# Performance work log

Hardware: AMD Instinct MI355X
Metric: run time of the kernel (lower is better)

Reference implementation:

```python
import jax, jax.numpy as jnp
import numpy as np

B, EEG_D, FMRI_D, BD, H, NC = 131072, 128, 64, 128, 4, 2
HD = BD // H  # head dim = 32
EPS = 1e-5

def layernorm(x, g, b):
    m = jnp.mean(x, axis=-1, keepdims=True)
    v = jnp.var(x, axis=-1, keepdims=True)
    return (x - m) * jax.lax.rsqrt(v + EPS) * g + b

def setup_inputs() -> dict:
    key = jax.random.key(0)
    ks = jax.random.split(key, 24)
    r = lambda i, shape, s=0.05: jax.random.normal(ks[i], shape, dtype=jnp.float32) * s
    return {
        'eeg_feats': jax.random.normal(ks[0], (B, EEG_D), dtype=jnp.float32),
        'fmri_feats': jax.random.normal(ks[1], (B, FMRI_D), dtype=jnp.float32),
        # projections (weights stored [in, out])
        'We': r(2, (EEG_D, BD)), 'be': jnp.zeros((BD,)),
        'ge': jnp.ones((BD,)), 'bge': jnp.zeros((BD,)),
        'Wf': r(3, (FMRI_D, BD)), 'bf': jnp.zeros((BD,)),
        'gf': jnp.ones((BD,)), 'bgf': jnp.zeros((BD,)),
        # multihead attention
        'Wq': r(4, (BD, BD)), 'bq': jnp.zeros((BD,)),
        'Wk': r(5, (BD, BD)), 'bk': jnp.zeros((BD,)),
        'Wv': r(6, (BD, BD)), 'bv': jnp.zeros((BD,)),
        'Wo': r(7, (BD, BD)), 'bo': jnp.zeros((BD,)),
        # learned fusion
        'fusion_logits': jnp.zeros((2,)),
        'temperature': jnp.ones(()),
        # classifier
        'Wc1': r(8, (BD, BD // 2)), 'bc1': jnp.zeros((BD // 2,)),
        'gc': jnp.ones((BD // 2,)), 'bgc': jnp.zeros((BD // 2,)),
        'Wc2': r(9, (BD // 2, NC)), 'bc2': jnp.zeros((NC,)),
    }

def reference(eeg_feats, fmri_feats, We, be, ge, bge, Wf, bf, gf, bgf,
              Wq, bq, Wk, bk, Wv, bv, Wo, bo, fusion_logits, temperature,
              Wc1, bc1, gc, bgc, Wc2, bc2):
    # modality projections: Linear + LN + GELU (dropout off at eval)
    eeg_p = jax.nn.gelu(layernorm(eeg_feats @ We + be, ge, bge), approximate=False)
    fmri_p = jax.nn.gelu(layernorm(fmri_feats @ Wf + bf, gf, bgf), approximate=False)

    # cross-attention: query = eeg_p (1 token), kv = [eeg_p, fmri_p] (2 tokens)
    seq = jnp.stack([eeg_p, fmri_p], axis=1)                 # [B, 2, BD]
    q = (eeg_p @ Wq + bq).reshape(B, H, HD)                  # [B, H, HD]
    k = (seq @ Wk + bk).reshape(B, 2, H, HD)
    v = (seq @ Wv + bv).reshape(B, 2, H, HD)
    scores = jnp.einsum('bhd,bkhd->bhk', q, k) / jnp.sqrt(jnp.float32(HD))
    attn = jax.nn.softmax(scores, axis=-1)                   # [B, H, 2]
    ctx = jnp.einsum('bhk,bkhd->bhd', attn, v).reshape(B, BD)
    eeg_enh = ctx @ Wo + bo                                  # [B, BD]

    # learned temperature-scaled fusion over [eeg_enhanced, fmri_proj]
    w = jax.nn.softmax(fusion_logits / temperature, axis=0)
    fused = w[0] * eeg_enh + w[1] * fmri_p                   # [B, BD]

    # classifier: Linear + LN + ReLU + Linear
    h = jax.nn.relu(layernorm(fused @ Wc1 + bc1, gc, bgc))
    logits = h @ Wc2 + bc2                                   # [B, NC]
    return logits
```

## Files before the change

kernel.cpp:

```cpp
#include <hip/hip_runtime.h>
#include <math.h>

#define EPS 1e-5f
#define SCALE 0.17677669529663687f

#define OFF_We  0
#define OFF_Wf  16384
#define OFF_Wq  24576
#define OFF_Wk  40960
#define OFF_Wv  57344
#define OFF_Wo  73728
#define OFF_Wc1 90112
#define PACK_TOTAL 98304

#define CHUNK 4096
#define NCHUNK 24
#define WAVES 16

typedef __bf16 bf16x8 __attribute__((ext_vector_type(8)));
typedef float f32x4 __attribute__((ext_vector_type(4)));
typedef unsigned short ushort_t;
typedef unsigned short ushortx4 __attribute__((ext_vector_type(4)));

__device__ __forceinline__ ushort_t f2bf(float x) {
    return __builtin_bit_cast(ushort_t, (__bf16)x);
}
__device__ __forceinline__ float bf2f(ushort_t v) {
    unsigned u = ((unsigned)v) << 16;
    return __builtin_bit_cast(float, u);
}

__device__ __forceinline__ ushort_t f2bf_sw(float x) {
    unsigned u = __builtin_bit_cast(unsigned, x);
    u = (u + 0x7fffu + ((u >> 16) & 1u)) >> 16;
    return (ushort_t)u;
}

#define DPPADD(x, ctrl) \
    ((x) + __builtin_bit_cast(float, __builtin_amdgcn_update_dpp( \
        __builtin_bit_cast(int, (x)), __builtin_bit_cast(int, (x)), (ctrl), 0xF, 0xF, false)))

__device__ __forceinline__ float rowsum16(float x) {
    x = DPPADD(x, 0x121);
    x = DPPADD(x, 0x122);
    x = DPPADD(x, 0x124);
    x = DPPADD(x, 0x128);
    return x;
}

__device__ __forceinline__ float gelu_fast(float x) {
    float x2 = x * x;
    float u = x * fmaf(0.07135481283f, x2, 1.5957691216f);
    float e = __expf(-u);
    return x * __builtin_amdgcn_rcpf(1.0f + e);
}

__global__ __launch_bounds__(256) void pack_all(
    const float* __restrict__ We, const float* __restrict__ Wf,
    const float* __restrict__ Wq, const float* __restrict__ Wk,
    const float* __restrict__ Wv, const float* __restrict__ Wo,
    const float* __restrict__ Wc1, ushort_t* __restrict__ ws)
{
    int o = blockIdx.x * 256 + threadIdx.x;
    if (o >= PACK_TOTAL) return;
    const float* W; int K, N, base;
    if (o < OFF_Wf)        { W = We;  K = 128; N = 128; base = OFF_We; }
    else if (o < OFF_Wq)   { W = Wf;  K = 64;  N = 128; base = OFF_Wf; }
    else if (o < OFF_Wk)   { W = Wq;  K = 128; N = 128; base = OFF_Wq; }
    else if (o < OFF_Wv)   { W = Wk;  K = 128; N = 128; base = OFF_Wk; }
    else if (o < OFF_Wo)   { W = Wv;  K = 128; N = 128; base = OFF_Wv; }
    else if (o < OFF_Wc1)  { W = Wo;  K = 128; N = 128; base = OFF_Wo; }
    else                   { W = Wc1; K = 128; N = 64;  base = OFF_Wc1; }
    int e = o - base;
    int j = e & 7, l = (e >> 3) & 63, rest = e >> 9;
    int KS = K >> 5;
    int s = rest % KS, t = rest / KS;
    int k = s * 32 + ((l >> 4) << 3) + j;
    int n = (t << 4) + (l & 15);
    ws[o] = f2bf_sw(W[k * N + n]);
}

template<int KS>
__device__ __forceinline__ void load_af(bf16x8 af[KS], const ushort_t* A, int lane)
{
    const int quad = lane >> 4, l16 = lane & 15;
    #pragma unroll
    for (int ks = 0; ks < KS; ++ks)
        af[ks] = *(const bf16x8*)(A + l16 * 136 + ks * 32 + quad * 8);
}

template<int KS, int NT>
__device__ __forceinline__ void mma_chunk(const bf16x8 af[KS], const ushort_t* sWb,
                                          f32x4* acc, int lane)
{
    #pragma unroll
    for (int t = 0; t < NT; ++t)
        #pragma unroll
        for (int ks = 0; ks < KS; ++ks) {
            bf16x8 bb = *(const bf16x8*)(sWb + ((t * KS + ks) * 64 + lane) * 8);
            acc[t] = __builtin_amdgcn_mfma_f32_16x16x32_bf16(af[ks], bb, acc[t], 0, 0, 0);
        }
}

__global__ __launch_bounds__(1024, 1) void fusion_stage(
    const float* __restrict__ eeg, const float* __restrict__ fmri,
    const float* __restrict__ be, const float* __restrict__ ge, const float* __restrict__ bge,
    const float* __restrict__ bfb, const float* __restrict__ gf, const float* __restrict__ bgf,
    const float* __restrict__ bq, const float* __restrict__ bk, const float* __restrict__ bv,
    const float* __restrict__ bo,
    const float* __restrict__ fusion_logits, const float* __restrict__ temperature,
    const float* __restrict__ bc1, const float* __restrict__ gc, const float* __restrict__ bgc,
    const float* __restrict__ Wc2, const float* __restrict__ bc2,
    const ushort_t* __restrict__ ws, float* __restrict__ out)
{
    __shared__ __align__(16) ushort_t sW[2][CHUNK];
    __shared__ __align__(16) ushort_t B1[WAVES][16 * 136];
    __shared__ __align__(16) ushort_t B2[WAVES][16 * 136];

    const int tid = threadIdx.x;
    const int wave = tid >> 6, lane = tid & 63;
    const int quad = lane >> 4, l16 = lane & 15;
    const int rowbase = blockIdx.x * (WAVES * 16) + wave * 16;
    ushort_t* b1 = B1[wave];
    ushort_t* b2 = B2[wave];

    auto prefetch = [&](int c) {
        if (wave < 8) {
            const char* g = (const char*)(ws + c * CHUNK) + wave * 1024 + lane * 16;
            char* l = (char*)(sW[c & 1]) + wave * 1024;
            __builtin_amdgcn_global_load_lds(
                (const __attribute__((address_space(1))) void*)g,
                (__attribute__((address_space(3))) void*)l, 16, 0, 0);
        }
    };

    int ck = 0;
    auto step = [&]() -> const ushort_t* {
        __syncthreads();
        if (ck + 1 < NCHUNK) prefetch(ck + 1);
        const ushort_t* p = sW[ck & 1];
        ++ck;
        return p;
    };

    prefetch(0);

    {
        const float4* src = (const float4*)(eeg + (size_t)rowbase * 128);
        #pragma unroll
        for (int i = 0; i < 8; ++i) {
            int idx = i * 64 + lane;
            float4 v = src[idx];
            int r = idx >> 5, k4 = (idx & 31) * 4;
            *(ushortx4*)&b1[r * 136 + k4] =
                (ushortx4){f2bf(v.x), f2bf(v.y), f2bf(v.z), f2bf(v.w)};
        }
        const float4* srcf = (const float4*)(fmri + (size_t)rowbase * 64);
        #pragma unroll
        for (int i = 0; i < 4; ++i) {
            int idx = i * 64 + lane;
            float4 v = srcf[idx];
            int r = idx >> 4, k4 = (idx & 15) * 4;
            *(ushortx4*)&b2[r * 136 + k4] =
                (ushortx4){f2bf(v.x), f2bf(v.y), f2bf(v.z), f2bf(v.w)};
        }
    }

    float meanS[4], rstdS[4];

    {
        bf16x8 afR[4]; load_af<4>(afR, b1, lane);
        f32x4 acc[8];
        #pragma unroll
        for (int nt = 0; nt < 8; ++nt) {
            float b = be[nt * 16 + l16];
            acc[nt] = (f32x4){b, b, b, b};
        }
        mma_chunk<4, 2>(afR, step(), acc + 0, lane);
        mma_chunk<4, 2>(afR, step(), acc + 2, lane);
        mma_chunk<4, 2>(afR, step(), acc + 4, lane);
        mma_chunk<4, 2>(afR, step(), acc + 6, lane);
        #pragma unroll
        for (int r = 0; r < 4; ++r) {
            float s = 0.f, ss = 0.f;
            #pragma unroll
            for (int nt = 0; nt < 8; ++nt) { float x = acc[nt][r]; s += x; ss = fmaf(x, x, ss); }
            s = rowsum16(s); ss = rowsum16(ss);
            float m = s * (1.f / 128.f);
            meanS[r] = m;
            rstdS[r] = rsqrtf(ss * (1.f / 128.f) - m * m + EPS);
        }
        #pragma unroll
        for (int nt = 0; nt < 8; ++nt) {
            float g = ge[nt * 16 + l16], bb = bge[nt * 16 + l16];
            #pragma unroll
            for (int r = 0; r < 4; ++r) {
                float x = (acc[nt][r] - meanS[r]) * rstdS[r] * g + bb;
                b1[(quad * 4 + r) * 136 + nt * 16 + l16] = f2bf(gelu_fast(x));
            }
        }
    }

    {
        bf16x8 afR[2]; load_af<2>(afR, b2, lane);
        f32x4 acc[8];
        #pragma unroll
        for (int nt = 0; nt < 8; ++nt) {
            float b = bfb[nt * 16 + l16];
            acc[nt] = (f32x4){b, b, b, b};
        }
        mma_chunk<2, 4>(afR, step(), acc + 0, lane);
        mma_chunk<2, 4>(afR, step(), acc + 4, lane);
        #pragma unroll
        for (int r = 0; r < 4; ++r) {
            float s = 0.f, ss = 0.f;
            #pragma unroll
            for (int nt = 0; nt < 8; ++nt) { float x = acc[nt][r]; s += x; ss = fmaf(x, x, ss); }
            s = rowsum16(s); ss = rowsum16(ss);
            float m = s * (1.f / 128.f);
            meanS[r] = m;
            rstdS[r] = rsqrtf(ss * (1.f / 128.f) - m * m + EPS);
        }
        #pragma unroll
        for (int nt = 0; nt < 8; ++nt) {
            float g = gf[nt * 16 + l16], bb = bgf[nt * 16 + l16];
            #pragma unroll
            for (int r = 0; r < 4; ++r) {
                float x = (acc[nt][r] - meanS[r]) * rstdS[r] * g + bb;
                b2[(quad * 4 + r) * 136 + nt * 16 + l16] = f2bf(gelu_fast(x));
            }
        }
    }

    bf16x8 afE[4]; load_af<4>(afE, b1, lane);
    bf16x8 afF[4]; load_af<4>(afF, b2, lane);

    f32x4 q[8];
    {
        #pragma unroll
        for (int nt = 0; nt < 8; ++nt) {
            float b = bq[nt * 16 + l16];
            q[nt] = (f32x4){b, b, b, b};
        }
        mma_chunk<4, 2>(afE, step(), q + 0, lane);
        mma_chunk<4, 2>(afE, step(), q + 2, lane);
        mma_chunk<4, 2>(afE, step(), q + 4, lane);
        mma_chunk<4, 2>(afE, step(), q + 6, lane);
    }

    float a0v[4][4];
    {
        float pd[4][4];
        #pragma unroll
        for (int h = 0; h < 4; ++h)
            #pragma unroll
            for (int r = 0; r < 4; ++r) pd[h][r] = 0.f;
        #pragma unroll
        for (int c = 0; c < 4; ++c) {
            const ushort_t* p = step();
            #pragma unroll
            for (int tl = 0; tl < 2; ++tl) {
                int nt = c * 2 + tl;
                f32x4 e = {0.f, 0.f, 0.f, 0.f}, f = {0.f, 0.f, 0.f, 0.f};
                #pragma unroll
                for (int ks = 0; ks < 4; ++ks) {
                    bf16x8 bb = *(const bf16x8*)(p + ((tl * 4 + ks) * 64 + lane) * 8);
                    e = __builtin_amdgcn_mfma_f32_16x16x32_bf16(afE[ks], bb, e, 0, 0, 0);
                    f = __builtin_amdgcn_mfma_f32_16x16x32_bf16(afF[ks], bb, f, 0, 0, 0);
                }
                int h = nt >> 1;
                #pragma unroll
                for (int r = 0; r < 4; ++r)
                    pd[h][r] = fmaf(q[nt][r], e[r] - f[r], pd[h][r]);
            }
        }
        #pragma unroll
        for (int h = 0; h < 4; ++h)
            #pragma unroll
            for (int r = 0; r < 4; ++r) {
                float d = rowsum16(pd[h][r]) * SCALE;
                a0v[h][r] = __builtin_amdgcn_rcpf(1.0f + __expf(-d));
            }
    }

    #pragma unroll
    for (int c = 0; c < 4; ++c) {
        const ushort_t* p = step();
        #pragma unroll
        for (int tl = 0; tl < 2; ++tl) {
            int nt = c * 2 + tl;
            float b = bv[nt * 16 + l16];
            f32x4 e = {b, b, b, b}, f = {b, b, b, b};
            #pragma unroll
            for (int ks = 0; ks < 4; ++ks) {
                bf16x8 bb = *(const bf16x8*)(p + ((tl * 4 + ks) * 64 + lane) * 8);
                e = __builtin_amdgcn_mfma_f32_16x16x32_bf16(afE[ks], bb, e, 0, 0, 0);
                f = __builtin_amdgcn_mfma_f32_16x16x32_bf16(afF[ks], bb, f, 0, 0, 0);
            }
            int h = nt >> 1;
            #pragma unroll
            for (int r = 0; r < 4; ++r) {
                float a0 = a0v[h][r];
                float c0 = a0 * e[r] + (1.0f - a0) * f[r];
                b1[(quad * 4 + r) * 136 + nt * 16 + l16] = f2bf(c0);
            }
        }
    }

    {
        bf16x8 afC[4]; load_af<4>(afC, b1, lane);
        f32x4 acc[8];
        #pragma unroll
        for (int nt = 0; nt < 8; ++nt) {
            float b = bo[nt * 16 + l16];
            acc[nt] = (f32x4){b, b, b, b};
        }
        mma_chunk<4, 2>(afC, step(), acc + 0, lane);
        mma_chunk<4, 2>(afC, step(), acc + 2, lane);
        mma_chunk<4, 2>(afC, step(), acc + 4, lane);
        mma_chunk<4, 2>(afC, step(), acc + 6, lane);
        float t = temperature[0];
        float dl = (fusion_logits[0] - fusion_logits[1]) / t;
        float w0 = __builtin_amdgcn_rcpf(1.0f + __expf(-dl));
        float w1 = 1.0f - w0;
        #pragma unroll
        for (int nt = 0; nt < 8; ++nt)
            #pragma unroll
            for (int r = 0; r < 4; ++r) {
                int off = (quad * 4 + r) * 136 + nt * 16 + l16;
                float fp = bf2f(b2[off]);
                b1[off] = f2bf(w0 * acc[nt][r] + w1 * fp);
            }
    }

    {
        bf16x8 afU[4]; load_af<4>(afU, b1, lane);
        f32x4 accH[4];
        #pragma unroll
        for (int nt = 0; nt < 4; ++nt) {
            float b = bc1[nt * 16 + l16];
            accH[nt] = (f32x4){b, b, b, b};
        }
        mma_chunk<4, 2>(afU, step(), accH + 0, lane);
        mma_chunk<4, 2>(afU, step(), accH + 2, lane);
        #pragma unroll
        for (int r = 0; r < 4; ++r) {
            float s = 0.f, ss = 0.f;
            #pragma unroll
            for (int nt = 0; nt < 4; ++nt) { float x = accH[nt][r]; s += x; ss = fmaf(x, x, ss); }
            s = rowsum16(s); ss = rowsum16(ss);
            float m = s * (1.f / 64.f);
            meanS[r] = m;
            rstdS[r] = rsqrtf(ss * (1.f / 64.f) - m * m + EPS);
        }
        float hv[4][4];
        #pragma unroll
        for (int nt = 0; nt < 4; ++nt) {
            float g = gc[nt * 16 + l16], bb = bgc[nt * 16 + l16];
            #pragma unroll
            for (int r = 0; r < 4; ++r) {
                float x = (accH[nt][r] - meanS[r]) * rstdS[r] * g + bb;
                hv[nt][r] = fmaxf(x, 0.0f);
            }
        }
        float w2v[4][2];
        #pragma unroll
        for (int nt = 0; nt < 4; ++nt) {
            float2 w = *(const float2*)&Wc2[(nt * 16 + l16) * 2];
            w2v[nt][0] = w.x; w2v[nt][1] = w.y;
        }
        float o0c = bc2[0], o1c = bc2[1];
        #pragma unroll
        for (int r = 0; r < 4; ++r) {
            float p0 = 0.f, p1 = 0.f;
            #pragma unroll
            for (int nt = 0; nt < 4; ++nt) {
                p0 = fmaf(hv[nt][r], w2v[nt][0], p0);
                p1 = fmaf(hv[nt][r], w2v[nt][1], p1);
            }
            p0 = rowsum16(p0); p1 = rowsum16(p1);
            if (l16 == 0) {
                int row = rowbase + quad * 4 + r;
                float2 o; o.x = p0 + o0c; o.y = p1 + o1c;
                *(float2*)&out[row * 2] = o;
            }
        }
    }
}

extern "C" void kernel_launch(void* const* d_in, const int* in_sizes, int n_in,
                              void* d_out, int out_size, void* d_ws, size_t ws_size,
                              hipStream_t stream) {
    const float* eeg  = (const float*)d_in[0];
    const float* fmri = (const float*)d_in[1];
    const float* We   = (const float*)d_in[2];
    const float* be   = (const float*)d_in[3];
    const float* ge   = (const float*)d_in[4];
    const float* bge  = (const float*)d_in[5];
    const float* Wf   = (const float*)d_in[6];
    const float* bf   = (const float*)d_in[7];
    const float* gf   = (const float*)d_in[8];
    const float* bgf  = (const float*)d_in[9];
    const float* Wq   = (const float*)d_in[10];
    const float* bq   = (const float*)d_in[11];
    const float* Wk   = (const float*)d_in[12];
    const float* bk   = (const float*)d_in[13];
    const float* Wv   = (const float*)d_in[14];
    const float* bv   = (const float*)d_in[15];
    const float* Wo   = (const float*)d_in[16];
    const float* bo   = (const float*)d_in[17];
    const float* fl   = (const float*)d_in[18];
    const float* temp = (const float*)d_in[19];
    const float* Wc1  = (const float*)d_in[20];
    const float* bc1  = (const float*)d_in[21];
    const float* gc   = (const float*)d_in[22];
    const float* bgc  = (const float*)d_in[23];
    const float* Wc2  = (const float*)d_in[24];
    const float* bc2  = (const float*)d_in[25];
    float* out = (float*)d_out;
    ushort_t* ws = (ushort_t*)d_ws;

    hipLaunchKernelGGL(pack_all, dim3((PACK_TOTAL + 255) / 256), dim3(256), 0, stream,
                       We, Wf, Wq, Wk, Wv, Wo, Wc1, ws);

    int B = in_sizes[0] / 128;
    int grid = B / (WAVES * 16);
    hipLaunchKernelGGL(fusion_stage, dim3(grid), dim3(1024), 0, stream,
                       eeg, fmri, be, ge, bge, bf, gf, bgf,
                       bq, bk, bv, bo, fl, temp, bc1, gc, bgc, Wc2, bc2,
                       ws, out);
}
```

Measured before the change: 216.6 us.

## Process 32 rows per wave with 8 waves to reuse weight fragments

Each wave now handles two 16-row tiles, and every B fragment read from LDS feeds two MFMAs instead of one. The block shrinks to 8 waves (512 threads) with the same rows per block, and all 8 waves take part in the weight prefetch. This halves LDS weight reads per row and halves the barriers per row, but doubles accumulator and fragment registers per wave, which risks spills or lower occupancy.

```diff
diff --git a/kernel.cpp b/kernel.cpp
--- a/kernel.cpp
+++ b/kernel.cpp
@@ -15,7 +15,7 @@
 
 #define CHUNK 4096
 #define NCHUNK 24
-#define WAVES 16
+#define WAVES 8
 
 typedef __bf16 bf16x8 __attribute__((ext_vector_type(8)));
 typedef float f32x4 __attribute__((ext_vector_type(4)));
@@ -90,19 +90,20 @@
 }
 
 template<int KS, int NT>
-__device__ __forceinline__ void mma_chunk(const bf16x8 af[KS], const ushort_t* sWb,
-                                          f32x4* acc, int lane)
+__device__ __forceinline__ void mma2(const bf16x8 a0[KS], const bf16x8 a1[KS],
+                                     const ushort_t* sWb, f32x4* c0, f32x4* c1, int lane)
 {
     #pragma unroll
     for (int t = 0; t < NT; ++t)
         #pragma unroll
         for (int ks = 0; ks < KS; ++ks) {
             bf16x8 bb = *(const bf16x8*)(sWb + ((t * KS + ks) * 64 + lane) * 8);
-            acc[t] = __builtin_amdgcn_mfma_f32_16x16x32_bf16(af[ks], bb, acc[t], 0, 0, 0);
-        }
-}
-
-__global__ __launch_bounds__(1024, 1) void fusion_stage(
+            c0[t] = __builtin_amdgcn_mfma_f32_16x16x32_bf16(a0[ks], bb, c0[t], 0, 0, 0);
+            c1[t] = __builtin_amdgcn_mfma_f32_16x16x32_bf16(a1[ks], bb, c1[t], 0, 0, 0);
+        }
+}
+
+__global__ __launch_bounds__(512, 1) void fusion_stage(
     const float* __restrict__ eeg, const float* __restrict__ fmri,
     const float* __restrict__ be, const float* __restrict__ ge, const float* __restrict__ bge,
     const float* __restrict__ bfb, const float* __restrict__ gf, const float* __restrict__ bgf,
@@ -114,24 +115,22 @@
     const ushort_t* __restrict__ ws, float* __restrict__ out)
 {
     __shared__ __align__(16) ushort_t sW[2][CHUNK];
-    __shared__ __align__(16) ushort_t B1[WAVES][16 * 136];
-    __shared__ __align__(16) ushort_t B2[WAVES][16 * 136];
+    __shared__ __align__(16) ushort_t B1[WAVES][32 * 136];
+    __shared__ __align__(16) ushort_t B2[WAVES][32 * 136];
 
     const int tid = threadIdx.x;
     const int wave = tid >> 6, lane = tid & 63;
     const int quad = lane >> 4, l16 = lane & 15;
-    const int rowbase = blockIdx.x * (WAVES * 16) + wave * 16;
+    const int rowbase = blockIdx.x * (WAVES * 32) + wave * 32;
     ushort_t* b1 = B1[wave];
     ushort_t* b2 = B2[wave];
 
     auto prefetch = [&](int c) {
-        if (wave < 8) {
-            const char* g = (const char*)(ws + c * CHUNK) + wave * 1024 + lane * 16;
-            char* l = (char*)(sW[c & 1]) + wave * 1024;
-            __builtin_amdgcn_global_load_lds(
-                (const __attribute__((address_space(1))) void*)g,
-                (__attribute__((address_space(3))) void*)l, 16, 0, 0);
-        }
+        const char* g = (const char*)(ws + c * CHUNK) + wave * 1024 + lane * 16;
+        char* l = (char*)(sW[c & 1]) + wave * 1024;
+        __builtin_amdgcn_global_load_lds(
+            (const __attribute__((address_space(1))) void*)g,
+            (__attribute__((address_space(3))) void*)l, 16, 0, 0);
     };
 
     int ck = 0;
@@ -148,7 +147,7 @@
     {
         const float4* src = (const float4*)(eeg + (size_t)rowbase * 128);
         #pragma unroll
-        for (int i = 0; i < 8; ++i) {
+        for (int i = 0; i < 16; ++i) {
             int idx = i * 64 + lane;
             float4 v = src[idx];
             int r = idx >> 5, k4 = (idx & 31) * 4;
@@ -157,7 +156,7 @@
         }
         const float4* srcf = (const float4*)(fmri + (size_t)rowbase * 64);
         #pragma unroll
-        for (int i = 0; i < 4; ++i) {
+        for (int i = 0; i < 8; ++i) {
             int idx = i * 64 + lane;
             float4 v = srcf[idx];
             int r = idx >> 4, k4 = (idx & 15) * 4;
@@ -166,121 +165,146 @@
         }
     }
 
-    float meanS[4], rstdS[4];
-
-    {
-        bf16x8 afR[4]; load_af<4>(afR, b1, lane);
-        f32x4 acc[8];
+    {
+        bf16x8 af0[4], af1[4];
+        load_af<4>(af0, b1, lane);
+        load_af<4>(af1, b1 + 16 * 136, lane);
+        f32x4 acc[2][8];
         #pragma unroll
         for (int nt = 0; nt < 8; ++nt) {
             float b = be[nt * 16 + l16];
-            acc[nt] = (f32x4){b, b, b, b};
-        }
-        mma_chunk<4, 2>(afR, step(), acc + 0, lane);
-        mma_chunk<4, 2>(afR, step(), acc + 2, lane);
-        mma_chunk<4, 2>(afR, step(), acc + 4, lane);
-        mma_chunk<4, 2>(afR, step(), acc + 6, lane);
-        #pragma unroll
-        for (int r = 0; r < 4; ++r) {
-            float s = 0.f, ss = 0.f;
-            #pragma unroll
-            for (int nt = 0; nt < 8; ++nt) { float x = acc[nt][r]; s += x; ss = fmaf(x, x, ss); }
-            s = rowsum16(s); ss = rowsum16(ss);
-            float m = s * (1.f / 128.f);
-            meanS[r] = m;
-            rstdS[r] = rsqrtf(ss * (1.f / 128.f) - m * m + EPS);
-        }
-        #pragma unroll
-        for (int nt = 0; nt < 8; ++nt) {
-            float g = ge[nt * 16 + l16], bb = bge[nt * 16 + l16];
+            acc[0][nt] = (f32x4){b, b, b, b};
+            acc[1][nt] = (f32x4){b, b, b, b};
+        }
+        mma2<4, 2>(af0, af1, step(), acc[0] + 0, acc[1] + 0, lane);
+        mma2<4, 2>(af0, af1, step(), acc[0] + 2, acc[1] + 2, lane);
+        mma2<4, 2>(af0, af1, step(), acc[0] + 4, acc[1] + 4, lane);
+        mma2<4, 2>(af0, af1, step(), acc[0] + 6, acc[1] + 6, lane);
+        #pragma unroll
+        for (int g = 0; g < 2; ++g) {
+            float meanS[4], rstdS[4];
             #pragma unroll
             for (int r = 0; r < 4; ++r) {
-                float x = (acc[nt][r] - meanS[r]) * rstdS[r] * g + bb;
-                b1[(quad * 4 + r) * 136 + nt * 16 + l16] = f2bf(gelu_fast(x));
-            }
-        }
-    }
-
-    {
-        bf16x8 afR[2]; load_af<2>(afR, b2, lane);
-        f32x4 acc[8];
+                float s = 0.f, ss = 0.f;
+                #pragma unroll
+                for (int nt = 0; nt < 8; ++nt) { float x = acc[g][nt][r]; s += x; ss = fmaf(x, x, ss); }
+                s = rowsum16(s); ss = rowsum16(ss);
+                float m = s * (1.f / 128.f);
+                meanS[r] = m;
+                rstdS[r] = rsqrtf(ss * (1.f / 128.f) - m * m + EPS);
+            }
+            #pragma unroll
+            for (int nt = 0; nt < 8; ++nt) {
+                float gg = ge[nt * 16 + l16], bb = bge[nt * 16 + l16];
+                #pragma unroll
+                for (int r = 0; r < 4; ++r) {
+                    float x = (acc[g][nt][r] - meanS[r]) * rstdS[r] * gg + bb;
+                    b1[(g * 16 + quad * 4 + r) * 136 + nt * 16 + l16] = f2bf(gelu_fast(x));
+                }
+            }
+        }
+    }
+
+    {
+        bf16x8 af0[2], af1[2];
+        load_af<2>(af0, b2, lane);
+        load_af<2>(af1, b2 + 16 * 136, lane);
+        f32x4 acc[2][8];
         #pragma unroll
         for (int nt = 0; nt < 8; ++nt) {
             float b = bfb[nt * 16 + l16];
-            acc[nt] = (f32x4){b, b, b, b};
-        }
-        mma_chunk<2, 4>(afR, step(), acc + 0, lane);
-        mma_chunk<2, 4>(afR, step(), acc + 4, lane);
-        #pragma unroll
-        for (int r = 0; r < 4; ++r) {
-            float s = 0.f, ss = 0.f;
-            #pragma unroll
-            for (int nt = 0; nt < 8; ++nt) { float x = acc[nt][r]; s += x; ss = fmaf(x, x, ss); }
-            s = rowsum16(s); ss = rowsum16(ss);
-            float m = s * (1.f / 128.f);
-            meanS[r] = m;
-            rstdS[r] = rsqrtf(ss * (1.f / 128.f) - m * m + EPS);
-        }
-        #pragma unroll
-        for (int nt = 0; nt < 8; ++nt) {
-            float g = gf[nt * 16 + l16], bb = bgf[nt * 16 + l16];
+            acc[0][nt] = (f32x4){b, b, b, b};
+            acc[1][nt] = (f32x4){b, b, b, b};
+        }
+        mma2<2, 4>(af0, af1, step(), acc[0] + 0, acc[1] + 0, lane);
+        mma2<2, 4>(af0, af1, step(), acc[0] + 4, acc[1] + 4, lane);
+        #pragma unroll
+        for (int g = 0; g < 2; ++g) {
+            float meanS[4], rstdS[4];
             #pragma unroll
             for (int r = 0; r < 4; ++r) {
-                float x = (acc[nt][r] - meanS[r]) * rstdS[r] * g + bb;
-                b2[(quad * 4 + r) * 136 + nt * 16 + l16] = f2bf(gelu_fast(x));
-            }
-        }
-    }
-
-    bf16x8 afE[4]; load_af<4>(afE, b1, lane);
-    bf16x8 afF[4]; load_af<4>(afF, b2, lane);
-
-    f32x4 q[8];
+                float s = 0.f, ss = 0.f;
+                #pragma unroll
+                for (int nt = 0; nt < 8; ++nt) { float x = acc[g][nt][r]; s += x; ss = fmaf(x, x, ss); }
+                s = rowsum16(s); ss = rowsum16(ss);
+                float m = s * (1.f / 128.f);
+                meanS[r] = m;
+                rstdS[r] = rsqrtf(ss * (1.f / 128.f) - m * m + EPS);
+            }
+            #pragma unroll
+            for (int nt = 0; nt < 8; ++nt) {
+                float gg = gf[nt * 16 + l16], bb = bgf[nt * 16 + l16];
+                #pragma unroll
+                for (int r = 0; r < 4; ++r) {
+                    float x = (acc[g][nt][r] - meanS[r]) * rstdS[r] * gg + bb;
+                    b2[(g * 16 + quad * 4 + r) * 136 + nt * 16 + l16] = f2bf(gelu_fast(x));
+                }
+            }
+        }
+    }
+
+    bf16x8 afE[2][4], afF[2][4];
+    load_af<4>(afE[0], b1, lane);
+    load_af<4>(afE[1], b1 + 16 * 136, lane);
+    load_af<4>(afF[0], b2, lane);
+    load_af<4>(afF[1], b2 + 16 * 136, lane);
+
+    f32x4 q[2][8];
     {
         #pragma unroll
         for (int nt = 0; nt < 8; ++nt) {
             float b = bq[nt * 16 + l16];
-            q[nt] = (f32x4){b, b, b, b};
-        }
-        mma_chunk<4, 2>(afE, step(), q + 0, lane);
-        mma_chunk<4, 2>(afE, step(), q + 2, lane);
-        mma_chunk<4, 2>(afE, step(), q + 4, lane);
-        mma_chunk<4, 2>(afE, step(), q + 6, lane);
-    }
-
-    float a0v[4][4];
-    {
-        float pd[4][4];
-        #pragma unroll
-        for (int h = 0; h < 4; ++h)
-            #pragma unroll
-            for (int r = 0; r < 4; ++r) pd[h][r] = 0.f;
+            q[0][nt] = (f32x4){b, b, b, b};
+            q[1][nt] = (f32x4){b, b, b, b};
+        }
+        mma2<4, 2>(afE[0], afE[1], step(), q[0] + 0, q[1] + 0, lane);
+        mma2<4, 2>(afE[0], afE[1], step(), q[0] + 2, q[1] + 2, lane);
+        mma2<4, 2>(afE[0], afE[1], step(), q[0] + 4, q[1] + 4, lane);
+        mma2<4, 2>(afE[0], afE[1], step(), q[0] + 6, q[1] + 6, lane);
+    }
+
+    float a0v[2][4][4];
+    {
+        float pd[2][4][4];
+        #pragma unroll
+        for (int g = 0; g < 2; ++g)
+            #pragma unroll
+            for (int h = 0; h < 4; ++h)
+                #pragma unroll
+                for (int r = 0; r < 4; ++r) pd[g][h][r] = 0.f;
         #pragma unroll
         for (int c = 0; c < 4; ++c) {
             const ushort_t* p = step();
             #pragma unroll
             for (int tl = 0; tl < 2; ++tl) {
                 int nt = c * 2 + tl;
-                f32x4 e = {0.f, 0.f, 0.f, 0.f}, f = {0.f, 0.f, 0.f, 0.f};
+                f32x4 e0 = {0.f, 0.f, 0.f, 0.f}, f0 = {0.f, 0.f, 0.f, 0.f};
+                f32x4 e1 = {0.f, 0.f, 0.f, 0.f}, f1 = {0.f, 0.f, 0.f, 0.f};
                 #pragma unroll
                 for (int ks = 0; ks < 4; ++ks) {
                     bf16x8 bb = *(const bf16x8*)(p + ((tl * 4 + ks) * 64 + lane) * 8);
-                    e = __builtin_amdgcn_mfma_f32_16x16x32_bf16(afE[ks], bb, e, 0, 0, 0);
-                    f = __builtin_amdgcn_mfma_f32_16x16x32_bf16(afF[ks], bb, f, 0, 0, 0);
+                    e0 = __builtin_amdgcn_mfma_f32_16x16x32_bf16(afE[0][ks], bb, e0, 0, 0, 0);
+                    f0 = __builtin_amdgcn_mfma_f32_16x16x32_bf16(afF[0][ks], bb, f0, 0, 0, 0);
+                    e1 = __builtin_amdgcn_mfma_f32_16x16x32_bf16(afE[1][ks], bb, e1, 0, 0, 0);
+                    f1 = __builtin_amdgcn_mfma_f32_16x16x32_bf16(afF[1][ks], bb, f1, 0, 0, 0);
                 }
                 int h = nt >> 1;
                 #pragma unroll
-                for (int r = 0; r < 4; ++r)
-                    pd[h][r] = fmaf(q[nt][r], e[r] - f[r], pd[h][r]);
-            }
-        }
-        #pragma unroll
-        for (int h = 0; h < 4; ++h)
-            #pragma unroll
-            for (int r = 0; r < 4; ++r) {
-                float d = rowsum16(pd[h][r]) * SCALE;
-                a0v[h][r] = __builtin_amdgcn_rcpf(1.0f + __expf(-d));
-            }
+                for (int r = 0; r < 4; ++r) {
+                    pd[0][h][r] = fmaf(q[0][nt][r], e0[r] - f0[r], pd[0][h][r]);
+                    pd[1][h][r] = fmaf(q[1][nt][r], e1[r] - f1[r], pd[1][h][r]);
+                }
+            }
+        }
+        #pragma unroll
+        for (int g = 0; g < 2; ++g)
+            #pragma unroll
+            for (int h = 0; h < 4; ++h)
+                #pragma unroll
+                for (int r = 0; r < 4; ++r) {
+                    float d = rowsum16(pd[g][h][r]) * SCALE;
+                    a0v[g][h][r] = __builtin_amdgcn_rcpf(1.0f + __expf(-d));
+                }
     }
 
     #pragma unroll
@@ -290,79 +314,73 @@
         for (int tl = 0; tl < 2; ++tl) {
             int nt = c * 2 + tl;
             float b = bv[nt * 16 + l16];
-            f32x4 e = {b, b, b, b}, f = {b, b, b, b};
+            f32x4 e0 = {b, b, b, b}, f0 = {b, b, b, b};
+            f32x4 e1 = {b, b, b, b}, f1 = {b, b, b, b};
             #pragma unroll
             for (int ks = 0; ks < 4; ++ks) {
                 bf16x8 bb = *(const bf16x8*)(p + ((tl * 4 + ks) * 64 + lane) * 8);
-                e = __builtin_amdgcn_mfma_f32_16x16x32_bf16(afE[ks], bb, e, 0, 0, 0);
-                f = __builtin_amdgcn_mfma_f32_16x16x32_bf16(afF[ks], bb, f, 0, 0, 0);
+                e0 = __builtin_amdgcn_mfma_f32_16x16x32_bf16(afE[0][ks], bb, e0, 0, 0, 0);
+                f0 = __builtin_amdgcn_mfma_f32_16x16x32_bf16(afF[0][ks], bb, f0, 0, 0, 0);
+                e1 = __builtin_amdgcn_mfma_f32_16x16x32_bf16(afE[1][ks], bb, e1, 0, 0, 0);
+                f1 = __builtin_amdgcn_mfma_f32_16x16x32_bf16(afF[1][ks], bb, f1, 0, 0, 0);
             }
             int h = nt >> 1;
             #pragma unroll
             for (int r = 0; r < 4; ++r) {
-                float a0 = a0v[h][r];
-                float c0 = a0 * e[r] + (1.0f - a0) * f[r];
+                float a00 = a0v[0][h][r];
+                float a01 = a0v[1][h][r];
+                float c0 = a00 * e0[r] + (1.0f - a00) * f0[r];
+                float c1 = a01 * e1[r] + (1.0f - a01) * f1[r];
                 b1[(quad * 4 + r) * 136 + nt * 16 + l16] = f2bf(c0);
-            }
-        }
-    }
-
-    {
-        bf16x8 afC[4]; load_af<4>(afC, b1, lane);
-        f32x4 acc[8];
+                b1[(16 + quad * 4 + r) * 136 + nt * 16 + l16] = f2bf(c1);
+            }
+        }
+    }
+
+    {
+        bf16x8 afC0[4], afC1[4];
+        load_af<4>(afC0, b1, lane);
+        load_af<4>(afC1, b1 + 16 * 136, lane);
+        f32x4 acc[2][8];
         #pragma unroll
         for (int nt = 0; nt < 8; ++nt) {
             float b = bo[nt * 16 + l16];
-            acc[nt] = (f32x4){b, b, b, b};
-        }
-        mma_chunk<4, 2>(afC, step(), acc + 0, lane);
-        mma_chunk<4, 2>(afC, step(), acc + 2, lane);
-        mma_chunk<4, 2>(afC, step(), acc + 4, lane);
-        mma_chunk<4, 2>(afC, step(), acc + 6, lane);
+            acc[0][nt] = (f32x4){b, b, b, b};
+            acc[1][nt] = (f32x4){b, b, b, b};
+        }
+        mma2<4, 2>(afC0, afC1, step(), acc[0] + 0, acc[1] + 0, lane);
+        mma2<4, 2>(afC0, afC1, step(), acc[0] + 2, acc[1] + 2, lane);
+        mma2<4, 2>(afC0, afC1, step(), acc[0] + 4, acc[1] + 4, lane);
+        mma2<4, 2>(afC0, afC1, step(), acc[0] + 6, acc[1] + 6, lane);
         float t = temperature[0];
         float dl = (fusion_logits[0] - fusion_logits[1]) / t;
         float w0 = __builtin_amdgcn_rcpf(1.0f + __expf(-dl));
         float w1 = 1.0f - w0;
         #pragma unroll
-        for (int nt = 0; nt < 8; ++nt)
-            #pragma unroll
-            for (int r = 0; r < 4; ++r) {
-                int off = (quad * 4 + r) * 136 + nt * 16 + l16;
-                float fp = bf2f(b2[off]);
-                b1[off] = f2bf(w0 * acc[nt][r] + w1 * fp);
-            }
-    }
-
-    {
-        bf16x8 afU[4]; load_af<4>(afU, b1, lane);
-        f32x4 accH[4];
+        for (int g = 0; g < 2; ++g)
+            #pragma unroll
+            for (int nt = 0; nt < 8; ++nt)
+                #pragma unroll
+                for (int r = 0; r < 4; ++r) {
+                    int off = (g * 16 + quad * 4 + r) * 136 + nt * 16 + l16;
+                    float fp = bf2f(b2[off]);
+                    b1[off] = f2bf(w0 * acc[g][nt][r] + w1 * fp);
+                }
+    }
+
+    {
+        bf16x8 afU0[4], afU1[4];
+        load_af<4>(afU0, b1, lane);
+        load_af<4>(afU1, b1 + 16 * 136, lane);
+        f32x4 accH[2][4];
         #pragma unroll
         for (int nt = 0; nt < 4; ++nt) {
             float b = bc1[nt * 16 + l16];
-            accH[nt] = (f32x4){b, b, b, b};
-        }
-        mma_chunk<4, 2>(afU, step(), accH + 0, lane);
-        mma_chunk<4, 2>(afU, step(), accH + 2, lane);
-        #pragma unroll
-        for (int r = 0; r < 4; ++r) {
-            float s = 0.f, ss = 0.f;
-            #pragma unroll
-            for (int nt = 0; nt < 4; ++nt) { float x = accH[nt][r]; s += x; ss = fmaf(x, x, ss); }
-            s = rowsum16(s); ss = rowsum16(ss);
-            float m = s * (1.f / 64.f);
-            meanS[r] = m;
-            rstdS[r] = rsqrtf(ss * (1.f / 64.f) - m * m + EPS);
-        }
-        float hv[4][4];
-        #pragma unroll
-        for (int nt = 0; nt < 4; ++nt) {
-            float g = gc[nt * 16 + l16], bb = bgc[nt * 16 + l16];
-            #pragma unroll
-            for (int r = 0; r < 4; ++r) {
-                float x = (accH[nt][r] - meanS[r]) * rstdS[r] * g + bb;
-                hv[nt][r] = fmaxf(x, 0.0f);
-            }
-        }
+            accH[0][nt] = (f32x4){b, b, b, b};
+            accH[1][nt] = (f32x4){b, b, b, b};
+        }
+        mma2<4, 2>(afU0, afU1, step(), accH[0] + 0, accH[1] + 0, lane);
+        mma2<4, 2>(afU0, afU1, step(), accH[0] + 2, accH[1] + 2, lane);
         float w2v[4][2];
         #pragma unroll
         for (int nt = 0; nt < 4; ++nt) {
@@ -371,18 +389,42 @@
         }
         float o0c = bc2[0], o1c = bc2[1];
         #pragma unroll
-        for (int r = 0; r < 4; ++r) {
-            float p0 = 0.f, p1 = 0.f;
+        for (int g = 0; g < 2; ++g) {
+            float meanS[4], rstdS[4];
+            #pragma unroll
+            for (int r = 0; r < 4; ++r) {
+                float s = 0.f, ss = 0.f;
+                #pragma unroll
+                for (int nt = 0; nt < 4; ++nt) { float x = accH[g][nt][r]; s += x; ss = fmaf(x, x, ss); }
+                s = rowsum16(s); ss = rowsum16(ss);
+                float m = s * (1.f / 64.f);
+                meanS[r] = m;
+                rstdS[r] = rsqrtf(ss * (1.f / 64.f) - m * m + EPS);
+            }
+            float hv[4][4];
             #pragma unroll
             for (int nt = 0; nt < 4; ++nt) {
-                p0 = fmaf(hv[nt][r], w2v[nt][0], p0);
-                p1 = fmaf(hv[nt][r], w2v[nt][1], p1);
-            }
-            p0 = rowsum16(p0); p1 = rowsum16(p1);
-            if (l16 == 0) {
-                int row = rowbase + quad * 4 + r;
-                float2 o; o.x = p0 + o0c; o.y = p1 + o1c;
-                *(float2*)&out[row * 2] = o;
+                float gg = gc[nt * 16 + l16], bb = bgc[nt * 16 + l16];
+                #pragma unroll
+                for (int r = 0; r < 4; ++r) {
+                    float x = (accH[g][nt][r] - meanS[r]) * rstdS[r] * gg + bb;
+                    hv[nt][r] = fmaxf(x, 0.0f);
+                }
+            }
+            #pragma unroll
+            for (int r = 0; r < 4; ++r) {
+                float p0 = 0.f, p1 = 0.f;
+                #pragma unroll
+                for (int nt = 0; nt < 4; ++nt) {
+                    p0 = fmaf(hv[nt][r], w2v[nt][0], p0);
+                    p1 = fmaf(hv[nt][r], w2v[nt][1], p1);
+                }
+                p0 = rowsum16(p0); p1 = rowsum16(p1);
+                if (l16 == 0) {
+                    int row = rowbase + g * 16 + quad * 4 + r;
+                    float2 o; o.x = p0 + o0c; o.y = p1 + o1c;
+                    *(float2*)&out[row * 2] = o;
+                }
             }
         }
     }
@@ -424,8 +466,8 @@
                        We, Wf, Wq, Wk, Wv, Wo, Wc1, ws);
 
     int B = in_sizes[0] / 128;
-    int grid = B / (WAVES * 16);
-    hipLaunchKernelGGL(fusion_stage, dim3(grid), dim3(1024), 0, stream,
+    int grid = B / (WAVES * 32);
+    hipLaunchKernelGGL(fusion_stage, dim3(grid), dim3(512), 0, stream,
                        eeg, fmri, be, ge, bge, bf, gf, bgf,
                        bq, bk, bv, bo, fl, temp, bc1, gc, bgc, Wc2, bc2,
                        ws, out);
```

Result: slower. 241.8 us (+11.7%).
